# Performance work log

Hardware: AMD Instinct MI355X
Metric: run time of the kernel (lower is better)

Reference implementation:

```python
import jax, jax.numpy as jnp
import numpy as np

N_F = 100000   # station (feature) nodes
N_H = 49152    # healpix nodes (12*4^6)
E = 400000     # edges per timestep
T_IN = 12
T_OUT = 12
H = 64         # hidden_size (must equal 64: cat with Linear(1,64) output)
A_H = 2 * H    # AttentionReadout hidden_size


def setup_inputs() -> dict:
    key = jax.random.key(0)
    ks = jax.random.split(key, 20)
    feat = jax.random.normal(ks[0], (N_F, T_IN, 1), dtype=jnp.float32)
    enc_src = jax.random.randint(ks[1], (E,), 0, N_F, dtype=jnp.int32)
    enc_dst = jax.random.randint(ks[2], (E,), 0, N_H, dtype=jnp.int32)
    dec_src = jax.random.randint(ks[3], (E,), 0, N_H, dtype=jnp.int32)
    dec_dst = jax.random.randint(ks[4], (E,), 0, N_F, dtype=jnp.int32)
    s = 0.05
    return {
        'feat': feat,
        'enc_src': enc_src, 'enc_dst': enc_dst,
        'dec_src': dec_src, 'dec_dst': dec_dst,
        # per-timestep encoder GraphConv(1 -> H) weights
        'W_enc': jax.random.normal(ks[5], (T_IN, 1, H), jnp.float32) * s,
        'b_enc': jnp.zeros((T_IN, H), jnp.float32),
        # MLP processor over time: Linear(T_IN -> T_OUT) + ReLU
        'W_proc': jax.random.normal(ks[6], (T_IN, T_OUT), jnp.float32) * s,
        'b_proc': jnp.zeros((T_OUT,), jnp.float32),
        # per-timestep decoder GraphConv(H -> H)
        'W_dec': jax.random.normal(ks[7], (T_OUT, H, H), jnp.float32) * s,
        'b_dec': jnp.zeros((T_OUT, H), jnp.float32),
        # decoder self.linears = Linear(1, 64)
        'W_lin': jax.random.normal(ks[8], (1, H), jnp.float32) * s,
        'b_lin': jnp.zeros((H,), jnp.float32),
        # AttentionReadout: score MLP (H -> 2H -> 1), output proj (H -> 1)
        'W_a1': jax.random.normal(ks[9], (H, A_H), jnp.float32) * s,
        'b_a1': jnp.zeros((A_H,), jnp.float32),
        'W_a2': jax.random.normal(ks[10], (A_H, 1), jnp.float32) * s,
        'b_a2': jnp.zeros((1,), jnp.float32),
        'W_o': jax.random.normal(ks[11], (H, 1), jnp.float32) * s,
        'b_o': jnp.zeros((1,), jnp.float32),
    }


def _gcn_norms(src, dst, n_src, n_dst):
    # DGL GraphConv norm='both': deg clamped to min 1, ^-0.5
    ones = jnp.ones(src.shape[0], jnp.float32)
    out_deg = jnp.maximum(jax.ops.segment_sum(ones, src, num_segments=n_src), 1.0)
    in_deg = jnp.maximum(jax.ops.segment_sum(ones, dst, num_segments=n_dst), 1.0)
    return out_deg ** -0.5, in_deg ** -0.5


def reference(feat, enc_src, enc_dst, dec_src, dec_dst,
              W_enc, b_enc, W_proc, b_proc, W_dec, b_dec,
              W_lin, b_lin, W_a1, b_a1, W_a2, b_a2, W_o, b_o):
    c_se, c_de = _gcn_norms(enc_src, enc_dst, N_F, N_H)
    c_sd, c_dd = _gcn_norms(dec_src, dec_dst, N_H, N_F)

    # ---- Graph_Encoder: per-t GraphConv(station -> healpix), 1 -> H ----
    x = jnp.nan_to_num(feat)                                  # [N_f, T_in, 1]
    msg = x * c_se[:, None, None]
    agg = jax.ops.segment_sum(msg[enc_src], enc_dst, num_segments=N_H)  # [N_h, T_in, 1]
    h_enc = jax.nn.leaky_relu(
        jnp.einsum('nti,tih->nth', agg * c_de[:, None, None], W_enc) + b_enc)  # [N_h, T_in, H]

    # ---- MLP_Processor: Linear over the time axis, T_in -> T_out, ReLU ----
    h_proc = jax.nn.relu(jnp.einsum('nth,to->noh', h_enc, W_proc)
                         + b_proc[:, None])                    # [N_h, T_out, H]
    h_proc_t = jnp.swapaxes(h_proc, 0, 1)                      # [T_out, N_h, H]

    # ---- Graph_Decoder: per-t GraphConv(healpix -> station) + Linear(prev) + AttentionReadout ----
    def step(y_prev, inp):
        h_t, W_t, b_t = inp                                    # h_t: [N_h, H]
        m = h_t * c_sd[:, None]
        a = jax.ops.segment_sum(m[dec_src], dec_dst, num_segments=N_F)  # [N_f, H]
        space1 = jax.nn.leaky_relu((a * c_dd[:, None]) @ W_t + b_t)     # [N_f, H]
        space2 = y_prev @ W_lin + b_lin                                 # [N_f, H]
        stacked = jnp.stack([space1, space2], axis=0)                   # [2, N_f, H]
        scores = jnp.tanh(stacked @ W_a1 + b_a1) @ W_a2 + b_a2          # [2, N_f, 1]
        alpha = jax.nn.softmax(scores, axis=0)
        states = jnp.sum(alpha * stacked, axis=0)                       # [N_f, H]
        y = states @ W_o + b_o                                          # [N_f, 1]
        return y, y

    y0 = x[:, -1]                                              # t{input_length-1}
    _, ys = jax.lax.scan(step, y0, (h_proc_t, W_dec, b_dec))
    return ys                                                  # [T_out, N_f, 1]
```

## Files before the change

kernel.cpp:

```cpp
#include <hip/hip_runtime.h>
#include <hip/hip_bf16.h>
#include <hip/hip_fp16.h>

#define NF 100000
#define NH 49152
#define EDG 400000
#define SLOTD 24
#define SLOTE 32

typedef __attribute__((ext_vector_type(8))) short short8;
typedef __attribute__((ext_vector_type(4))) float float4v;
typedef unsigned short u16;
typedef unsigned int u32;

__device__ __forceinline__ u16 f2b(float x) {
    u32 u = __float_as_uint(x);
    u32 r = u + 0x7FFFu + ((u >> 16) & 1u);
    return (u16)(r >> 16);
}
__device__ __forceinline__ __half2 h2(u32 v) { union { u32 u; __half2 h; } c; c.u = v; return c.h; }
__device__ __forceinline__ float fast_tanh(float x) {
    float ex = __expf(2.0f * x);
    return 1.0f - 2.0f / (ex + 1.0f);
}

#define PN1 (NF * 12)
#define PN2 (NH * SLOTE)
#define PN3 298304
#define PN4 384
__global__ void prefill(u32* __restrict__ csrD32, u32* __restrict__ csrE,
                        u32* __restrict__ degcnt, u32* __restrict__ mzero, int zstride) {
    int i = blockIdx.x * 256 + threadIdx.x;
    if (i < PN1) csrD32[i] = ((u32)NH << 16) | (u32)NH;
    else if (i < PN1 + PN2) csrE[i - PN1] = 0u;
    else if (i < PN1 + PN2 + PN3) degcnt[i - PN1 - PN2] = 0u;
    else if (i < PN1 + PN2 + PN3 + PN4) {
        int j = i - PN1 - PN2 - PN3;
        mzero[(j >> 7) * (size_t)zstride + (j & 127)] = 0u;
    }
}

__global__ void fill_slotted(const int* __restrict__ enc_src, const int* __restrict__ enc_dst,
                             const int* __restrict__ dec_src, const int* __restrict__ dec_dst,
                             int* __restrict__ cntD, u16* __restrict__ csrD, float* __restrict__ deg_sd,
                             int* __restrict__ cntE, u32* __restrict__ csrE, float* __restrict__ deg_se) {
    int e = blockIdx.x * 256 + threadIdx.x;
    if (e >= EDG) return;
    int ds = dec_src[e], dd = dec_dst[e];
    int i1 = atomicAdd(&cntD[dd], 1);
    if (i1 < SLOTD) csrD[(size_t)dd * SLOTD + i1] = (u16)ds;
    atomicAdd(&deg_sd[ds], 1.0f);
    int es = enc_src[e], ed = enc_dst[e];
    int i2 = atomicAdd(&cntE[ed], 1);
    if (i2 < SLOTE) csrE[(size_t)ed * SLOTE + i2] = (u32)es;
    atomicAdd(&deg_se[es], 1.0f);
}

__global__ void prep_small(const float* __restrict__ W_dec, const float* __restrict__ W_a1,
                           u16* __restrict__ fragWdec, u16* __restrict__ fragWa1,
                           const float* __restrict__ W_lin, const float* __restrict__ b_lin,
                           const float* __restrict__ b_a1, const float* __restrict__ W_o,
                           float* __restrict__ uvs) {
    const int b = blockIdx.x;
    if (b < 28) {
        int gid = b * 256 + threadIdx.x;
        if (gid >= 7168) return;
        int L = gid & 63;
        int f = gid >> 6;
        int q = L >> 4, cb = L & 15;
        if (f < 96) {
            int fr = f & 7;
            int c = fr >> 1, kc = fr & 1;
            int k0 = kc * 32 + q * 8;
            int nn = c * 16 + cb;
            int t = f >> 3;
            #pragma unroll
            for (int j = 0; j < 8; ++j)
                fragWdec[(f * 64 + L) * 8 + j] = f2b(W_dec[t * 4096 + (k0 + j) * 64 + nn]);
        } else {
            int fr = f - 96;
            int c2 = fr >> 1, kc = fr & 1;
            int k0 = kc * 32 + q * 8;
            int nn = c2 * 16 + cb;
            #pragma unroll
            for (int j = 0; j < 8; ++j)
                fragWa1[(fr * 64 + L) * 8 + j] = f2b(W_a1[(k0 + j) * 128 + nn]);
        }
    } else {
        int k = threadIdx.x;
        if (k < 128) {
            float su = 0.f, sv = 0.f;
            for (int h = 0; h < 64; ++h) {
                su = fmaf(W_lin[h], W_a1[h * 128 + k], su);
                sv = fmaf(b_lin[h], W_a1[h * 128 + k], sv);
            }
            uvs[k] = su;
            uvs[128 + k] = sv + b_a1[k];
            if (k == 0) {
                float a = 0.f, bb = 0.f;
                for (int h = 0; h < 64; ++h) {
                    a = fmaf(W_lin[h], W_o[h], a);
                    bb = fmaf(b_lin[h], W_o[h], bb);
                }
                uvs[256] = a;
                uvs[257] = bb;
            }
        }
    }
}

__global__ void build_gtab(const float* __restrict__ uvs, const float* __restrict__ W_a2,
                           float* __restrict__ gtab) {
    int i = blockIdx.x * 256 + threadIdx.x;
    if (i > 16384) return;
    float y = fmaf((float)i, 1.f / 256.f, -32.f);
    float s = 0.f;
    for (int k = 0; k < 128; ++k)
        s = fmaf(fast_tanh(fmaf(y, uvs[k], uvs[128 + k])), W_a2[k], s);
    gtab[i] = s;
}

__global__ __launch_bounds__(256) void enc_gather(const float* __restrict__ feat,
                                                  const float* __restrict__ deg_se,
                                                  const int* __restrict__ cntE,
                                                  const u32* __restrict__ csrE,
                                                  float* __restrict__ agg) {
    const int tid = threadIdx.x, lane = tid & 63, wid = tid >> 6;
    const int grp = lane >> 2, l = lane & 3;
    const int dst = blockIdx.x * 64 + wid * 16 + grp;
    int cnt = cntE[dst];
    if (cnt > SLOTE) cnt = SLOTE;
    const u32* cp = csrE + (size_t)dst * SLOTE;
    float4 a = {0.f, 0.f, 0.f, 0.f};
    if (l < 3) {
        for (int e = 0; e < cnt; e += 4) {
            u32 s0 = cp[e], s1 = cp[e + 1], s2 = cp[e + 2], s3 = cp[e + 3];
            float c0 = rsqrtf(fmaxf(deg_se[s0], 1.0f));
            float c1 = (e + 1 < cnt) ? rsqrtf(fmaxf(deg_se[s1], 1.0f)) : 0.f;
            float c2 = (e + 2 < cnt) ? rsqrtf(fmaxf(deg_se[s2], 1.0f)) : 0.f;
            float c3 = (e + 3 < cnt) ? rsqrtf(fmaxf(deg_se[s3], 1.0f)) : 0.f;
            float4 w0 = *(const float4*)(feat + (size_t)s0 * 12 + l * 4);
            float4 w1 = *(const float4*)(feat + (size_t)s1 * 12 + l * 4);
            float4 w2 = *(const float4*)(feat + (size_t)s2 * 12 + l * 4);
            float4 w3 = *(const float4*)(feat + (size_t)s3 * 12 + l * 4);
            w0.x = (w0.x != w0.x) ? 0.f : w0.x; w0.y = (w0.y != w0.y) ? 0.f : w0.y;
            w0.z = (w0.z != w0.z) ? 0.f : w0.z; w0.w = (w0.w != w0.w) ? 0.f : w0.w;
            w1.x = (w1.x != w1.x) ? 0.f : w1.x; w1.y = (w1.y != w1.y) ? 0.f : w1.y;
            w1.z = (w1.z != w1.z) ? 0.f : w1.z; w1.w = (w1.w != w1.w) ? 0.f : w1.w;
            w2.x = (w2.x != w2.x) ? 0.f : w2.x; w2.y = (w2.y != w2.y) ? 0.f : w2.y;
            w2.z = (w2.z != w2.z) ? 0.f : w2.z; w2.w = (w2.w != w2.w) ? 0.f : w2.w;
            w3.x = (w3.x != w3.x) ? 0.f : w3.x; w3.y = (w3.y != w3.y) ? 0.f : w3.y;
            w3.z = (w3.z != w3.z) ? 0.f : w3.z; w3.w = (w3.w != w3.w) ? 0.f : w3.w;
            a.x = fmaf(w0.x, c0, fmaf(w1.x, c1, fmaf(w2.x, c2, fmaf(w3.x, c3, a.x))));
            a.y = fmaf(w0.y, c0, fmaf(w1.y, c1, fmaf(w2.y, c2, fmaf(w3.y, c3, a.y))));
            a.z = fmaf(w0.z, c0, fmaf(w1.z, c1, fmaf(w2.z, c2, fmaf(w3.z, c3, a.z))));
            a.w = fmaf(w0.w, c0, fmaf(w1.w, c1, fmaf(w2.w, c2, fmaf(w3.w, c3, a.w))));
        }
    }
    *(float4*)(agg + (size_t)dst * 16 + l * 4) = a;
}

__global__ void make_all(const float* __restrict__ agg, const int* __restrict__ cntE,
                         const float* __restrict__ deg_sd, const float* __restrict__ W_enc,
                         const float* __restrict__ b_enc, const float* __restrict__ W_proc,
                         const float* __restrict__ b_proc, u16* __restrict__ m, size_t cstride) {
    int gid = blockIdx.x * 256 + threadIdx.x;
    if (gid >= NH * 64) return;
    int n = gid >> 6, h = gid & 63;
    float cde = rsqrtf(fmaxf((float)cntE[n], 1.0f));
    float csd = rsqrtf(fmaxf(deg_sd[n], 1.0f));
    float he[12];
    #pragma unroll
    for (int ti = 0; ti < 12; ++ti) {
        float a = agg[n * 16 + ti] * cde;
        float x = fmaf(a, W_enc[ti * 64 + h], b_enc[ti * 64 + h]);
        he[ti] = x > 0.f ? x : 0.01f * x;
    }
    #pragma unroll
    for (int c = 0; c < 3; ++c) {
        u16 r[4];
        #pragma unroll
        for (int tt = 0; tt < 4; ++tt) {
            int t = c * 4 + tt;
            float s = b_proc[t];
            #pragma unroll
            for (int ti = 0; ti < 12; ++ti) s = fmaf(he[ti], W_proc[ti * 12 + t], s);
            s = fmaxf(s, 0.f) * csd;
            r[tt] = __half_as_ushort(__float2half(s));
        }
        u32 o0 = ((u32)r[1] << 16) | r[0];
        u32 o1 = ((u32)r[3] << 16) | r[2];
        u32* dst = (u32*)(m + c * cstride + (size_t)n * 256 + h * 4);
        dst[0] = o0; dst[1] = o1;
    }
}

__global__ void make_chunk(const float* __restrict__ agg, const int* __restrict__ cntE,
                           const float* __restrict__ deg_sd, const float* __restrict__ W_enc,
                           const float* __restrict__ b_enc, const float* __restrict__ W_proc,
                           const float* __restrict__ b_proc, u16* __restrict__ m, int t0) {
    int gid = blockIdx.x * 256 + threadIdx.x;
    if (gid >= NH * 64) return;
    int n = gid >> 6, h = gid & 63;
    float cde = rsqrtf(fmaxf((float)cntE[n], 1.0f));
    float csd = rsqrtf(fmaxf(deg_sd[n], 1.0f));
    float he[12];
    #pragma unroll
    for (int ti = 0; ti < 12; ++ti) {
        float a = agg[n * 16 + ti] * cde;
        float x = fmaf(a, W_enc[ti * 64 + h], b_enc[ti * 64 + h]);
        he[ti] = x > 0.f ? x : 0.01f * x;
    }
    u16 r[4];
    #pragma unroll
    for (int tt = 0; tt < 4; ++tt) {
        int t = t0 + tt;
        float s = b_proc[t];
        #pragma unroll
        for (int ti = 0; ti < 12; ++ti) s = fmaf(he[ti], W_proc[ti * 12 + t], s);
        s = fmaxf(s, 0.f) * csd;
        r[tt] = __half_as_ushort(__float2half(s));
    }
    u32 o0 = ((u32)r[1] << 16) | r[0];
    u32 o1 = ((u32)r[3] << 16) | r[2];
    u32* dst = (u32*)(m + (size_t)n * 256 + h * 4);
    dst[0] = o0; dst[1] = o1;
}

__global__ __launch_bounds__(256) void dec_batch(
    const u16* __restrict__ mbase, const int* __restrict__ cntD, const u16* __restrict__ csrD,
    const u16* __restrict__ fragWdec, const u16* __restrict__ fragWa1,
    const float* __restrict__ b_dec, const float* __restrict__ b_a1,
    const float* __restrict__ W_a2, const float* __restrict__ W_o,
    float* __restrict__ S1, float* __restrict__ PW, int t0p, size_t mstride) {
    __shared__ __align__(16) u16 zs[22528];

    const u16* m = mbase + (size_t)blockIdx.y * mstride;
    const int t0 = t0p + blockIdx.y * 4;
    const int tid = threadIdx.x, lane = tid & 63, wid = tid >> 6;
    const int nw = blockIdx.x * 64 + wid * 16;
    const int g16 = lane >> 4, c16 = lane & 15;
    u16* zw0 = zs + wid * 5632;

    int cdw[4]; float cdd[4];
    uint4 q[4][3];
    #pragma unroll
    for (int k = 0; k < 4; ++k) {
        int n = nw + g16 * 4 + k;
        bool v = (n < NF);
        int nn = v ? n : 0;
        int cd = cntD[nn];
        cdd[k] = v ? rsqrtf(fmaxf((float)cd, 1.0f)) : 0.f;
        cdw[k] = v ? (cd > SLOTD ? SLOTD : cd) : 0;
        const uint4* cp4 = (const uint4*)(csrD + (size_t)nn * SLOTD);
        q[k][0] = cp4[0]; q[k][1] = cp4[1]; q[k][2] = cp4[2];
    }
    int cdmax = max(max(cdw[0], cdw[1]), max(cdw[2], cdw[3]));

    __half2 acc[4][8];
    #pragma unroll
    for (int k = 0; k < 4; ++k)
        #pragma unroll
        for (int i = 0; i < 8; ++i)
            acc[k][i] = __half2{__half(0.f), __half(0.f)};

    const u16* mrow = m + c16 * 16;
    #pragma unroll
    for (int it = 0; it < 6; ++it) {
        if (it >= 2 && !__any(it * 4 < cdmax)) break;
        #pragma unroll
        for (int k = 0; k < 4; ++k) {
            if (it * 4 < cdw[k]) {
                u32 lo = (it & 1) ? q[k][it >> 1].z : q[k][it >> 1].x;
                u32 hi = (it & 1) ? q[k][it >> 1].w : q[k][it >> 1].y;
                int s0 = (int)(lo & 0xFFFF), s1 = (int)(lo >> 16);
                int s2 = (int)(hi & 0xFFFF), s3 = (int)(hi >> 16);
                const uint4* r0 = (const uint4*)(mrow + (size_t)s0 * 256);
                const uint4* r1 = (const uint4*)(mrow + (size_t)s1 * 256);
                const uint4* r2 = (const uint4*)(mrow + (size_t)s2 * 256);
                const uint4* r3 = (const uint4*)(mrow + (size_t)s3 * 256);
                uint4 A0 = r0[0], B0 = r0[1];
                uint4 A1 = r1[0], B1 = r1[1];
                uint4 A2 = r2[0], B2 = r2[1];
                uint4 A3 = r3[0], B3 = r3[1];
                acc[k][0] = __hadd2(acc[k][0], __hadd2(__hadd2(h2(A0.x), h2(A1.x)), __hadd2(h2(A2.x), h2(A3.x))));
                acc[k][1] = __hadd2(acc[k][1], __hadd2(__hadd2(h2(A0.y), h2(A1.y)), __hadd2(h2(A2.y), h2(A3.y))));
                acc[k][2] = __hadd2(acc[k][2], __hadd2(__hadd2(h2(A0.z), h2(A1.z)), __hadd2(h2(A2.z), h2(A3.z))));
                acc[k][3] = __hadd2(acc[k][3], __hadd2(__hadd2(h2(A0.w), h2(A1.w)), __hadd2(h2(A2.w), h2(A3.w))));
                acc[k][4] = __hadd2(acc[k][4], __hadd2(__hadd2(h2(B0.x), h2(B1.x)), __hadd2(h2(B2.x), h2(B3.x))));
                acc[k][5] = __hadd2(acc[k][5], __hadd2(__hadd2(h2(B0.y), h2(B1.y)), __hadd2(h2(B2.y), h2(B3.y))));
                acc[k][6] = __hadd2(acc[k][6], __hadd2(__hadd2(h2(B0.z), h2(B1.z)), __hadd2(h2(B2.z), h2(B3.z))));
                acc[k][7] = __hadd2(acc[k][7], __hadd2(__hadd2(h2(B0.w), h2(B1.w)), __hadd2(h2(B2.w), h2(B3.w))));
            }
        }
    }

    #pragma unroll
    for (int k = 0; k < 4; ++k) {
        int j = g16 * 4 + k;
        float s = cdd[k];
        #pragma unroll
        for (int p = 0; p < 2; ++p) {
            float2 c0 = __half22float2(acc[k][0 * 2 + p]);
            float2 c1 = __half22float2(acc[k][1 * 2 + p]);
            float2 c2 = __half22float2(acc[k][2 * 2 + p]);
            float2 c3 = __half22float2(acc[k][3 * 2 + p]);
            u32 oA0 = ((u32)f2b(c1.x * s) << 16) | f2b(c0.x * s);
            u32 oA1 = ((u32)f2b(c3.x * s) << 16) | f2b(c2.x * s);
            u32 oB0 = ((u32)f2b(c1.y * s) << 16) | f2b(c0.y * s);
            u32 oB1 = ((u32)f2b(c3.y * s) << 16) | f2b(c2.y * s);
            u32* dA = (u32*)(zw0 + (2 * p) * 1408 + j * 88 + c16 * 4);
            u32* dB = (u32*)(zw0 + (2 * p + 1) * 1408 + j * 88 + c16 * 4);
            dA[0] = oA0; dA[1] = oA1;
            dB[0] = oB0; dB[1] = oB1;
        }
    }
    asm volatile("s_waitcnt lgkmcnt(0)" ::: "memory");

    for (int tt = 0; tt < 4; ++tt) {
        const int t = t0 + tt;
        u16* zw = zw0 + tt * 1408;
        const u16* ab = zw + c16 * 88 + g16 * 8;
        short8 a0 = *(const short8*)ab;
        short8 a1 = *(const short8*)(ab + 32);

        const u16* fw = fragWdec + (size_t)t * 4096;
        float4v C1[4];
        #pragma unroll
        for (int cc = 0; cc < 4; ++cc) {
            float4v z4 = {0.f, 0.f, 0.f, 0.f};
            short8 b0 = *(const short8*)(fw + (cc * 2 + 0) * 512 + lane * 8);
            short8 b1 = *(const short8*)(fw + (cc * 2 + 1) * 512 + lane * 8);
            z4 = __builtin_amdgcn_mfma_f32_16x16x32_bf16(a0, b0, z4, 0, 0, 0);
            C1[cc] = __builtin_amdgcn_mfma_f32_16x16x32_bf16(a1, b1, z4, 0, 0, 0);
        }

        float pw[4] = {0.f, 0.f, 0.f, 0.f};
        #pragma unroll
        for (int cc = 0; cc < 4; ++cc) {
            float bt = b_dec[t * 64 + cc * 16 + c16];
            float wo = W_o[cc * 16 + c16];
            #pragma unroll
            for (int r = 0; r < 4; ++r) {
                float xx = C1[cc][r] + bt;
                float sp = xx > 0.f ? xx : 0.01f * xx;
                pw[r] = fmaf(sp, wo, pw[r]);
                zw[(g16 * 4 + r) * 88 + cc * 16 + c16] = f2b(sp);
            }
        }
        asm volatile("s_waitcnt lgkmcnt(0)" ::: "memory");
        short8 sa0 = *(const short8*)ab;
        short8 sa1 = *(const short8*)(ab + 32);

        float4v C2[8];
        #pragma unroll
        for (int cc = 0; cc < 8; ++cc) {
            float4v z4 = {0.f, 0.f, 0.f, 0.f};
            short8 b0 = *(const short8*)(fragWa1 + (cc * 2 + 0) * 512 + lane * 8);
            short8 b1 = *(const short8*)(fragWa1 + (cc * 2 + 1) * 512 + lane * 8);
            z4 = __builtin_amdgcn_mfma_f32_16x16x32_bf16(sa0, b0, z4, 0, 0, 0);
            C2[cc] = __builtin_amdgcn_mfma_f32_16x16x32_bf16(sa1, b1, z4, 0, 0, 0);
        }

        float p1[4] = {0.f, 0.f, 0.f, 0.f};
        #pragma unroll
        for (int cc = 0; cc < 8; ++cc) {
            int k = cc * 16 + c16;
            float ba = b_a1[k], wa = W_a2[k];
            #pragma unroll
            for (int r = 0; r < 4; ++r)
                p1[r] = fmaf(fast_tanh(C2[cc][r] + ba), wa, p1[r]);
        }

        #pragma unroll
        for (int mm = 1; mm < 16; mm <<= 1) {
            #pragma unroll
            for (int r = 0; r < 4; ++r) {
                p1[r] += __shfl_xor(p1[r], mm);
                pw[r] += __shfl_xor(pw[r], mm);
            }
        }

        if (c16 == 0) {
            #pragma unroll
            for (int r = 0; r < 4; ++r) {
                int n = nw + g16 * 4 + r;
                if (n < NF) {
                    S1[(size_t)t * NF + n] = p1[r];
                    PW[(size_t)t * NF + n] = pw[r];
                }
            }
        }
    }
}

__global__ __launch_bounds__(256) void dec_scan(
    const float* __restrict__ S1, const float* __restrict__ PW,
    const float* __restrict__ gtab, const float* __restrict__ uvs,
    const float* __restrict__ feat, const float* __restrict__ b_a2p,
    const float* __restrict__ b_op, float* __restrict__ out) {
    const int n = blockIdx.x * 256 + threadIdx.x;
    if (n >= NF) return;
    float s1v[12], pwv[12];
    #pragma unroll
    for (int t = 0; t < 12; ++t) {
        s1v[t] = S1[(size_t)t * NF + n];
        pwv[t] = PW[(size_t)t * NF + n];
    }
    const float wlo = uvs[256], blo = uvs[257], ba2 = b_a2p[0], bo = b_op[0];
    float yp = feat[n * 12 + 11];
    yp = (yp != yp) ? 0.f : yp;
    #pragma unroll
    for (int t = 0; t < 12; ++t) {
        float xf = fminf(fmaxf(fmaf(yp, 256.f, 8192.f), 0.f), 16383.f);
        int idx = (int)xf;
        float fr = xf - (float)idx;
        float g0 = gtab[idx], g1 = gtab[idx + 1];
        float p2 = fmaf(g1 - g0, fr, g0);
        float s1s = s1v[t] + ba2, s2s = p2 + ba2;
        float mx = fmaxf(s1s, s2s);
        float e1 = __expf(s1s - mx), e2 = __expf(s2s - mx);
        float y = (e1 * pwv[t] + e2 * fmaf(wlo, yp, blo)) / (e1 + e2) + bo;
        out[(size_t)t * NF + n] = y;
        yp = y;
    }
}

extern "C" void kernel_launch(void* const* d_in, const int* in_sizes, int n_in,
                              void* d_out, int out_size, void* d_ws, size_t ws_size,
                              hipStream_t stream) {
    const float* feat   = (const float*)d_in[0];
    const int* enc_src  = (const int*)d_in[1];
    const int* enc_dst  = (const int*)d_in[2];
    const int* dec_src  = (const int*)d_in[3];
    const int* dec_dst  = (const int*)d_in[4];
    const float* W_enc  = (const float*)d_in[5];
    const float* b_enc  = (const float*)d_in[6];
    const float* W_proc = (const float*)d_in[7];
    const float* b_proc = (const float*)d_in[8];
    const float* W_dec  = (const float*)d_in[9];
    const float* b_dec  = (const float*)d_in[10];
    const float* W_lin  = (const float*)d_in[11];
    const float* b_lin  = (const float*)d_in[12];
    const float* W_a1   = (const float*)d_in[13];
    const float* b_a1   = (const float*)d_in[14];
    const float* W_a2   = (const float*)d_in[15];
    const float* b_a2   = (const float*)d_in[16];
    const float* W_o    = (const float*)d_in[17];
    const float* b_o    = (const float*)d_in[18];
    float* out = (float*)d_out;

    float* W = (float*)d_ws;
    float* deg_se   = W;
    float* deg_sd   = W + 100000;
    int*   cntD     = (int*)(W + 149152);
    int*   cntE     = (int*)(W + 249152);
    float* uvs      = W + 298304;
    u16*   fragWdec = (u16*)(W + 298624);
    u16*   fragWa1  = (u16*)(W + 323200);
    float* agg      = W + 327296;
    float* S1       = W + 1113728;
    float* PW       = W + 2313728;
    u16*   csrD     = (u16*)(W + 3513728);
    u32*   csrE     = (u32*)(W + 4713728);
    float* gtab     = W + 6286592;
    u16*   m_ws     = (u16*)(W + 6303104);

    const size_t CSTRIDE = (size_t)(NH + 1) * 256;
    const size_t need_full = ((size_t)6303104 + 3 * CSTRIDE / 2) * 4;
    const bool full = ws_size >= need_full;
    const int zstride = full ? (int)(CSTRIDE / 2) : 0;

    const int PTOT = PN1 + PN2 + PN3 + PN4;
    prefill<<<(PTOT + 255) / 256, 256, 0, stream>>>((u32*)csrD, csrE, (u32*)W,
                                                    (u32*)m_ws + (size_t)NH * 128, zstride);
    fill_slotted<<<(EDG + 255) / 256, 256, 0, stream>>>(enc_src, enc_dst, dec_src, dec_dst,
                                                        cntD, csrD, deg_sd, cntE, csrE, deg_se);
    prep_small<<<29, 256, 0, stream>>>(W_dec, W_a1, fragWdec, fragWa1,
                                       W_lin, b_lin, b_a1, W_o, uvs);
    build_gtab<<<65, 256, 0, stream>>>(uvs, W_a2, gtab);
    enc_gather<<<NH / 64, 256, 0, stream>>>(feat, deg_se, cntE, csrE, agg);

    const int dec_grid = (NF + 63) / 64;
    if (full) {
        make_all<<<(NH * 64) / 256, 256, 0, stream>>>(agg, cntE, deg_sd, W_enc, b_enc,
                                                      W_proc, b_proc, m_ws, CSTRIDE);
        dec_batch<<<dim3(dec_grid, 3), 256, 0, stream>>>(m_ws, cntD, csrD, fragWdec, fragWa1,
                                                         b_dec, b_a1, W_a2, W_o, S1, PW,
                                                         0, CSTRIDE);
    } else {
        for (int c = 0; c < 3; ++c) {
            make_chunk<<<(NH * 64) / 256, 256, 0, stream>>>(agg, cntE, deg_sd, W_enc, b_enc,
                                                            W_proc, b_proc, m_ws, 4 * c);
            dec_batch<<<dim3(dec_grid, 1), 256, 0, stream>>>(m_ws, cntD, csrD, fragWdec, fragWa1,
                                                             b_dec, b_a1, W_a2, W_o, S1, PW,
                                                             4 * c, 0);
        }
    }
    dec_scan<<<(NF + 255) / 256, 256, 0, stream>>>(S1, PW, gtab, uvs, feat, b_a2, b_o, out);
}
```

Before: 418.2 us.

## Cut dec_batch register and LDS use to raise occupancy

Adds launch_bounds(256,4) and shrinks the LDS row pitch from 88 to 72 halves, reducing per-block shared memory. The CSR index loads are now staged, fetching one uint4 at a time only when degrees require it, so twelve uint4 registers per thread drop to four. The attention MLP MFMA is split into two halves so only four accumulator tiles are live at once. The goal is more resident waves to hide gather latency, at the cost of possible spills under the forced bound and a new bank-conflict pattern with the 72 pitch.

New measurement: 399.1 us. 1.05x faster.

```diff
diff --git a/kernel.cpp b/kernel.cpp
--- a/kernel.cpp
+++ b/kernel.cpp
@@ -227,33 +227,53 @@
     dst[0] = o0; dst[1] = o1;
 }
 
-__global__ __launch_bounds__(256) void dec_batch(
+__device__ __forceinline__ void acc4(__half2* a8, const u16* mrow, u32 lo, u32 hi) {
+    int s0 = (int)(lo & 0xFFFF), s1 = (int)(lo >> 16);
+    int s2 = (int)(hi & 0xFFFF), s3 = (int)(hi >> 16);
+    const uint4* r0 = (const uint4*)(mrow + (size_t)s0 * 256);
+    const uint4* r1 = (const uint4*)(mrow + (size_t)s1 * 256);
+    const uint4* r2 = (const uint4*)(mrow + (size_t)s2 * 256);
+    const uint4* r3 = (const uint4*)(mrow + (size_t)s3 * 256);
+    uint4 A0 = r0[0], B0 = r0[1];
+    uint4 A1 = r1[0], B1 = r1[1];
+    uint4 A2 = r2[0], B2 = r2[1];
+    uint4 A3 = r3[0], B3 = r3[1];
+    a8[0] = __hadd2(a8[0], __hadd2(__hadd2(h2(A0.x), h2(A1.x)), __hadd2(h2(A2.x), h2(A3.x))));
+    a8[1] = __hadd2(a8[1], __hadd2(__hadd2(h2(A0.y), h2(A1.y)), __hadd2(h2(A2.y), h2(A3.y))));
+    a8[2] = __hadd2(a8[2], __hadd2(__hadd2(h2(A0.z), h2(A1.z)), __hadd2(h2(A2.z), h2(A3.z))));
+    a8[3] = __hadd2(a8[3], __hadd2(__hadd2(h2(A0.w), h2(A1.w)), __hadd2(h2(A2.w), h2(A3.w))));
+    a8[4] = __hadd2(a8[4], __hadd2(__hadd2(h2(B0.x), h2(B1.x)), __hadd2(h2(B2.x), h2(B3.x))));
+    a8[5] = __hadd2(a8[5], __hadd2(__hadd2(h2(B0.y), h2(B1.y)), __hadd2(h2(B2.y), h2(B3.y))));
+    a8[6] = __hadd2(a8[6], __hadd2(__hadd2(h2(B0.z), h2(B1.z)), __hadd2(h2(B2.z), h2(B3.z))));
+    a8[7] = __hadd2(a8[7], __hadd2(__hadd2(h2(B0.w), h2(B1.w)), __hadd2(h2(B2.w), h2(B3.w))));
+}
+
+__global__ __launch_bounds__(256, 4) void dec_batch(
     const u16* __restrict__ mbase, const int* __restrict__ cntD, const u16* __restrict__ csrD,
     const u16* __restrict__ fragWdec, const u16* __restrict__ fragWa1,
     const float* __restrict__ b_dec, const float* __restrict__ b_a1,
     const float* __restrict__ W_a2, const float* __restrict__ W_o,
     float* __restrict__ S1, float* __restrict__ PW, int t0p, size_t mstride) {
-    __shared__ __align__(16) u16 zs[22528];
+    __shared__ __align__(16) u16 zs[18432];
 
     const u16* m = mbase + (size_t)blockIdx.y * mstride;
     const int t0 = t0p + blockIdx.y * 4;
     const int tid = threadIdx.x, lane = tid & 63, wid = tid >> 6;
     const int nw = blockIdx.x * 64 + wid * 16;
     const int g16 = lane >> 4, c16 = lane & 15;
-    u16* zw0 = zs + wid * 5632;
-
-    int cdw[4]; float cdd[4];
-    uint4 q[4][3];
+    u16* zw0 = zs + wid * 4608;
+
+    int cdw[4]; float cdd[4]; int nnv[4];
+    uint4 qa[4];
     #pragma unroll
     for (int k = 0; k < 4; ++k) {
         int n = nw + g16 * 4 + k;
         bool v = (n < NF);
-        int nn = v ? n : 0;
-        int cd = cntD[nn];
+        nnv[k] = v ? n : 0;
+        int cd = cntD[nnv[k]];
         cdd[k] = v ? rsqrtf(fmaxf((float)cd, 1.0f)) : 0.f;
         cdw[k] = v ? (cd > SLOTD ? SLOTD : cd) : 0;
-        const uint4* cp4 = (const uint4*)(csrD + (size_t)nn * SLOTD);
-        q[k][0] = cp4[0]; q[k][1] = cp4[1]; q[k][2] = cp4[2];
+        qa[k] = *(const uint4*)(csrD + (size_t)nnv[k] * SLOTD);
     }
     int cdmax = max(max(cdw[0], cdw[1]), max(cdw[2], cdw[3]));
 
@@ -266,32 +286,23 @@
 
     const u16* mrow = m + c16 * 16;
     #pragma unroll
-    for (int it = 0; it < 6; ++it) {
-        if (it >= 2 && !__any(it * 4 < cdmax)) break;
-        #pragma unroll
-        for (int k = 0; k < 4; ++k) {
-            if (it * 4 < cdw[k]) {
-                u32 lo = (it & 1) ? q[k][it >> 1].z : q[k][it >> 1].x;
-                u32 hi = (it & 1) ? q[k][it >> 1].w : q[k][it >> 1].y;
-                int s0 = (int)(lo & 0xFFFF), s1 = (int)(lo >> 16);
-                int s2 = (int)(hi & 0xFFFF), s3 = (int)(hi >> 16);
-                const uint4* r0 = (const uint4*)(mrow + (size_t)s0 * 256);
-                const uint4* r1 = (const uint4*)(mrow + (size_t)s1 * 256);
-                const uint4* r2 = (const uint4*)(mrow + (size_t)s2 * 256);
-                const uint4* r3 = (const uint4*)(mrow + (size_t)s3 * 256);
-                uint4 A0 = r0[0], B0 = r0[1];
-                uint4 A1 = r1[0], B1 = r1[1];
-                uint4 A2 = r2[0], B2 = r2[1];
-                uint4 A3 = r3[0], B3 = r3[1];
-                acc[k][0] = __hadd2(acc[k][0], __hadd2(__hadd2(h2(A0.x), h2(A1.x)), __hadd2(h2(A2.x), h2(A3.x))));
-                acc[k][1] = __hadd2(acc[k][1], __hadd2(__hadd2(h2(A0.y), h2(A1.y)), __hadd2(h2(A2.y), h2(A3.y))));
-                acc[k][2] = __hadd2(acc[k][2], __hadd2(__hadd2(h2(A0.z), h2(A1.z)), __hadd2(h2(A2.z), h2(A3.z))));
-                acc[k][3] = __hadd2(acc[k][3], __hadd2(__hadd2(h2(A0.w), h2(A1.w)), __hadd2(h2(A2.w), h2(A3.w))));
-                acc[k][4] = __hadd2(acc[k][4], __hadd2(__hadd2(h2(B0.x), h2(B1.x)), __hadd2(h2(B2.x), h2(B3.x))));
-                acc[k][5] = __hadd2(acc[k][5], __hadd2(__hadd2(h2(B0.y), h2(B1.y)), __hadd2(h2(B2.y), h2(B3.y))));
-                acc[k][6] = __hadd2(acc[k][6], __hadd2(__hadd2(h2(B0.z), h2(B1.z)), __hadd2(h2(B2.z), h2(B3.z))));
-                acc[k][7] = __hadd2(acc[k][7], __hadd2(__hadd2(h2(B0.w), h2(B1.w)), __hadd2(h2(B2.w), h2(B3.w))));
-            }
+    for (int k = 0; k < 4; ++k) if (cdw[k] > 0) acc4(acc[k], mrow, qa[k].x, qa[k].y);
+    #pragma unroll
+    for (int k = 0; k < 4; ++k) if (cdw[k] > 4) acc4(acc[k], mrow, qa[k].z, qa[k].w);
+    if (__any(cdmax > 8)) {
+        #pragma unroll
+        for (int k = 0; k < 4; ++k) if (cdw[k] > 8) qa[k] = *(const uint4*)(csrD + (size_t)nnv[k] * SLOTD + 8);
+        #pragma unroll
+        for (int k = 0; k < 4; ++k) if (cdw[k] > 8) acc4(acc[k], mrow, qa[k].x, qa[k].y);
+        #pragma unroll
+        for (int k = 0; k < 4; ++k) if (cdw[k] > 12) acc4(acc[k], mrow, qa[k].z, qa[k].w);
+        if (__any(cdmax > 16)) {
+            #pragma unroll
+            for (int k = 0; k < 4; ++k) if (cdw[k] > 16) qa[k] = *(const uint4*)(csrD + (size_t)nnv[k] * SLOTD + 16);
+            #pragma unroll
+            for (int k = 0; k < 4; ++k) if (cdw[k] > 16) acc4(acc[k], mrow, qa[k].x, qa[k].y);
+            #pragma unroll
+            for (int k = 0; k < 4; ++k) if (cdw[k] > 20) acc4(acc[k], mrow, qa[k].z, qa[k].w);
         }
     }
 
@@ -309,8 +320,8 @@
             u32 oA1 = ((u32)f2b(c3.x * s) << 16) | f2b(c2.x * s);
             u32 oB0 = ((u32)f2b(c1.y * s) << 16) | f2b(c0.y * s);
             u32 oB1 = ((u32)f2b(c3.y * s) << 16) | f2b(c2.y * s);
-            u32* dA = (u32*)(zw0 + (2 * p) * 1408 + j * 88 + c16 * 4);
-            u32* dB = (u32*)(zw0 + (2 * p + 1) * 1408 + j * 88 + c16 * 4);
+            u32* dA = (u32*)(zw0 + (2 * p) * 1152 + j * 72 + c16 * 4);
+            u32* dB = (u32*)(zw0 + (2 * p + 1) * 1152 + j * 72 + c16 * 4);
             dA[0] = oA0; dA[1] = oA1;
             dB[0] = oB0; dB[1] = oB1;
         }
@@ -319,8 +330,8 @@
 
     for (int tt = 0; tt < 4; ++tt) {
         const int t = t0 + tt;
-        u16* zw = zw0 + tt * 1408;
-        const u16* ab = zw + c16 * 88 + g16 * 8;
+        u16* zw = zw0 + tt * 1152;
+        const u16* ab = zw + c16 * 72 + g16 * 8;
         short8 a0 = *(const short8*)ab;
         short8 a1 = *(const short8*)(ab + 32);
 
@@ -345,31 +356,34 @@
                 float xx = C1[cc][r] + bt;
                 float sp = xx > 0.f ? xx : 0.01f * xx;
                 pw[r] = fmaf(sp, wo, pw[r]);
-                zw[(g16 * 4 + r) * 88 + cc * 16 + c16] = f2b(sp);
+                zw[(g16 * 4 + r) * 72 + cc * 16 + c16] = f2b(sp);
             }
         }
         asm volatile("s_waitcnt lgkmcnt(0)" ::: "memory");
         short8 sa0 = *(const short8*)ab;
         short8 sa1 = *(const short8*)(ab + 32);
 
-        float4v C2[8];
-        #pragma unroll
-        for (int cc = 0; cc < 8; ++cc) {
-            float4v z4 = {0.f, 0.f, 0.f, 0.f};
-            short8 b0 = *(const short8*)(fragWa1 + (cc * 2 + 0) * 512 + lane * 8);
-            short8 b1 = *(const short8*)(fragWa1 + (cc * 2 + 1) * 512 + lane * 8);
-            z4 = __builtin_amdgcn_mfma_f32_16x16x32_bf16(sa0, b0, z4, 0, 0, 0);
-            C2[cc] = __builtin_amdgcn_mfma_f32_16x16x32_bf16(sa1, b1, z4, 0, 0, 0);
-        }
-
         float p1[4] = {0.f, 0.f, 0.f, 0.f};
         #pragma unroll
-        for (int cc = 0; cc < 8; ++cc) {
-            int k = cc * 16 + c16;
-            float ba = b_a1[k], wa = W_a2[k];
-            #pragma unroll
-            for (int r = 0; r < 4; ++r)
-                p1[r] = fmaf(fast_tanh(C2[cc][r] + ba), wa, p1[r]);
+        for (int half = 0; half < 2; ++half) {
+            float4v C2[4];
+            #pragma unroll
+            for (int cc = 0; cc < 4; ++cc) {
+                int c8 = half * 4 + cc;
+                float4v z4 = {0.f, 0.f, 0.f, 0.f};
+                short8 b0 = *(const short8*)(fragWa1 + (c8 * 2 + 0) * 512 + lane * 8);
+                short8 b1 = *(const short8*)(fragWa1 + (c8 * 2 + 1) * 512 + lane * 8);
+                z4 = __builtin_amdgcn_mfma_f32_16x16x32_bf16(sa0, b0, z4, 0, 0, 0);
+                C2[cc] = __builtin_amdgcn_mfma_f32_16x16x32_bf16(sa1, b1, z4, 0, 0, 0);
+            }
+            #pragma unroll
+            for (int cc = 0; cc < 4; ++cc) {
+                int k = (half * 4 + cc) * 16 + c16;
+                float ba = b_a1[k], wa = W_a2[k];
+                #pragma unroll
+                for (int r = 0; r < 4; ++r)
+                    p1[r] = fmaf(fast_tanh(C2[cc][r] + ba), wa, p1[r]);
+            }
         }
 
         #pragma unroll
```
